# Kernel optimization log

Hardware: AMD Instinct MI355X
Metric: run time of the kernel (lower is better)

Reference implementation:

```python
import jax, jax.numpy as jnp
import numpy as np

NEG_INF = -9e15
ALPHA = 0.2  # LeakyReLU negative slope

N, IN_F, OUT_F = 8192, 512, 64


def setup_inputs() -> dict:
    key = jax.random.key(0)
    k1, k2, k3, k4 = jax.random.split(key, 4)
    input = jax.random.normal(k1, (N, IN_F), dtype=jnp.float32)
    adj = jax.random.randint(k2, (N, N), 0, 2, dtype=jnp.int32)
    init_range = float(np.sqrt(6.0 / (IN_F + OUT_F)))
    W = jax.random.uniform(k3, (IN_F, OUT_F), dtype=jnp.float32,
                           minval=-init_range, maxval=init_range)
    a_range = float(np.sqrt(6.0 / (2 * OUT_F + 1)))
    a = jax.random.uniform(k4, (2 * OUT_F, 1), dtype=jnp.float32,
                           minval=-a_range, maxval=a_range)
    return {"input": input, "adj": adj, "W": W, "a": a}


def reference(input, adj, W, a):
    h = input @ W                      # [N, F']
    a_left, a_right = a[:OUT_F], a[OUT_F:]   # each [F', 1]
    att_l = h @ a_left                 # [N, 1]
    att_r = h @ a_right                # [N, 1]
    e = jax.nn.leaky_relu(att_l + att_r.T, negative_slope=ALPHA)  # [N, N]
    e = jnp.where(adj == 0, jnp.float32(NEG_INF), e)
    attention = jax.nn.softmax(e, axis=1)
    # dropout is identity in eval mode (training=False)
    h_prime = attention @ h            # [N, F']
    return jax.nn.elu(h_prime)         # concat=True -> ELU activation
```

## Files before the change

kernel.cpp:

```cpp
#include <hip/hip_runtime.h>
#include <stdint.h>

#define ALPHA 0.2f
#define LOG2E 1.44269504088896340736f

typedef __attribute__((ext_vector_type(8))) short bf16x8;
typedef __attribute__((ext_vector_type(4))) float f32x4;

__device__ __forceinline__ unsigned short f2bf(float f) {
    unsigned u = __builtin_bit_cast(unsigned, f);
    u += 0x7fffu + ((u >> 16) & 1u);
    return (unsigned short)(u >> 16);
}
__device__ __forceinline__ float bf2f(unsigned short h) {
    unsigned u = ((unsigned)h) << 16;
    return __builtin_bit_cast(float, u);
}
__device__ __forceinline__ unsigned f2ord(float f) {
    unsigned b = __builtin_bit_cast(unsigned, f);
    return (b & 0x80000000u) ? ~b : (b | 0x80000000u);
}
__device__ __forceinline__ float ord2f(unsigned k) {
    unsigned b = (k & 0x80000000u) ? (k & 0x7fffffffu) : ~k;
    return __builtin_bit_cast(float, b);
}

__global__ __launch_bounds__(256) void gat_h(
    const float* __restrict__ input, const float* __restrict__ W,
    float* __restrict__ h)
{
    __shared__ float x_lds[16 * 128];
    const int tid = threadIdx.x;
    const int i0  = (blockIdx.x >> 2) * 16;
    const int k0  = (blockIdx.x & 3) * 128;

    {
        const int r  = tid >> 4;
        const int jc = (tid & 15) * 8;
        const float* src = input + (size_t)(i0 + r) * 512 + k0 + jc;
        *(f32x4*)&x_lds[r * 128 + jc]     = *(const f32x4*)src;
        *(f32x4*)&x_lds[r * 128 + jc + 4] = *(const f32x4*)(src + 4);
    }
    __syncthreads();

    const int c = tid & 63;
    const int w = tid >> 6;
    float acc[4] = {0.f, 0.f, 0.f, 0.f};
    const float* Wc = W + (size_t)k0 * 64 + c;
    #pragma unroll 4
    for (int kk = 0; kk < 128; kk += 4) {
        const float w0 = Wc[(kk+0)*64], w1 = Wc[(kk+1)*64];
        const float w2 = Wc[(kk+2)*64], w3 = Wc[(kk+3)*64];
        #pragma unroll
        for (int ri = 0; ri < 4; ++ri) {
            const f32x4 x = *(const f32x4*)&x_lds[(w + 4*ri) * 128 + kk];
            acc[ri] += x.x * w0 + x.y * w1 + x.z * w2 + x.w * w3;
        }
    }
    #pragma unroll
    for (int ri = 0; ri < 4; ++ri)
        unsafeAtomicAdd(&h[(size_t)(i0 + w + 4*ri) * 64 + c], acc[ri]);
}

__global__ __launch_bounds__(256) void gat_aux(
    const float* __restrict__ h, const float* __restrict__ a,
    float* __restrict__ attL, float* __restrict__ attR,
    unsigned short* __restrict__ hPack, unsigned* __restrict__ wsR)
{
    __shared__ float hl[32 * 64];
    __shared__ unsigned rmax;
    const int tid = threadIdx.x;
    const int j0  = blockIdx.x * 32;
    if (tid == 0) rmax = 0u;

    {
        const float* src = h + (size_t)j0 * 64 + tid * 8;
        *(f32x4*)&hl[tid * 8]     = *(const f32x4*)src;
        *(f32x4*)&hl[tid * 8 + 4] = *(const f32x4*)(src + 4);
    }
    __syncthreads();

    {
        const int row = tid >> 3;
        const int cs  = (tid & 7) * 8;
        float pL = 0.f, pR = 0.f;
        #pragma unroll
        for (int u = 0; u < 8; ++u) {
            const float hv = hl[row * 64 + cs + u];
            pL += hv * a[cs + u];
            pR += hv * a[64 + cs + u];
        }
        pL += __shfl_xor(pL, 1, 64); pR += __shfl_xor(pR, 1, 64);
        pL += __shfl_xor(pL, 2, 64); pR += __shfl_xor(pR, 2, 64);
        pL += __shfl_xor(pL, 4, 64); pR += __shfl_xor(pR, 4, 64);
        if ((tid & 7) == 0) {
            attL[j0 + row] = pL;
            attR[j0 + row] = pR;
            atomicMax(&rmax, f2ord(pR));
        }
    }

    {
        const int g = tid >> 6;
        const int l = tid & 63;
        const int m = l & 15;
        const int q = l >> 4;
        bf16x8 v;
        #pragma unroll
        for (int u = 0; u < 8; ++u)
            v[u] = (short)f2bf(hl[(q * 8 + u) * 64 + g * 16 + m]);
        *(bf16x8*)&hPack[(size_t)(blockIdx.x * 4 + g) * 512 + l * 8] = v;
    }

    __syncthreads();
    if (tid == 0) atomicMax(wsR, rmax);
}

__global__ __launch_bounds__(256, 8) void gat_attn(
    const int* __restrict__ adj,
    const float* __restrict__ attL, const float* __restrict__ attR,
    const unsigned short* __restrict__ hPack, const unsigned* __restrict__ wsR,
    float* __restrict__ outAcc, float* __restrict__ lAcc)
{
    __shared__ unsigned smem[4096];
    __shared__ float l_lds[64];
    const int tid  = threadIdx.x;
    const int lane = tid & 63;
    const int wq   = tid >> 6;
    const int m    = lane & 15;
    const int quad = lane >> 4;
    const int ti   = blockIdx.x >> 2;
    const int q4   = blockIdx.x & 3;
    const int i0   = ti * 16;
    const int jc0  = q4 * 64 + wq * 16;

    {
        const int r    = tid >> 4;
        const int lidx = (tid & 3) * 16 + r;
        const int t    = (tid & 15) >> 2;
        unsigned char* bb = (unsigned char*)smem;
        const int* src = adj + (size_t)(i0 + r) * 8192 + q4 * 2048 + (tid & 15) * 8;
        #pragma unroll 4
        for (int it = 0; it < 16; ++it) {
            const int4 v0 = *(const int4*)(src + it * 128);
            const int4 v1 = *(const int4*)(src + it * 128 + 4);
            unsigned b = 0;
            b |= (v0.x != 0) << 0; b |= (v0.y != 0) << 1;
            b |= (v0.z != 0) << 2; b |= (v0.w != 0) << 3;
            b |= (v1.x != 0) << 4; b |= (v1.y != 0) << 5;
            b |= (v1.z != 0) << 6; b |= (v1.w != 0) << 7;
            bb[((((it >> 2) * 1024) + (it & 3) * 64 + lidx) << 2) + t] = (unsigned char)b;
        }
    }
    __syncthreads();

    unsigned abw[4];
    #pragma unroll
    for (int g4 = 0; g4 < 4; ++g4)
        abw[g4] = smem[wq * 1024 + g4 * 64 + lane];

    const float R   = ord2f(*wsR);
    const float a_l = attL[i0 + m];
    const float t0  = a_l + R;
    const float M   = fmaxf(t0, ALPHA * t0);
    const float mc  = M * LOG2E;

    const float*          ar_p = attR + jc0 * 32 + quad * 8;
    const unsigned short* hp_p = hPack + (size_t)jc0 * 4 * 512 + lane * 8;

    f32x4 acc[4];
    #pragma unroll
    for (int g = 0; g < 4; ++g) acc[g] = (f32x4){0.f, 0.f, 0.f, 0.f};
    float lsum = 0.f;

    #pragma unroll
    for (int jg = 0; jg < 4; ++jg) {
        const unsigned ab = abw[jg];
        #pragma unroll
        for (int t = 0; t < 4; ++t) {
            const int s = jg * 4 + t;
            const f32x4 r0 = *(const f32x4*)(ar_p + s * 32);
            const f32x4 r1 = *(const f32x4*)(ar_p + s * 32 + 4);
            bf16x8 B[4];
            #pragma unroll
            for (int g = 0; g < 4; ++g)
                B[g] = *(const bf16x8*)(hp_p + (size_t)(s * 4 + g) * 512);

            const unsigned bits = (ab >> (t * 8)) & 0xffu;
            const float tv[8] = { a_l + r0.x, a_l + r0.y, a_l + r0.z, a_l + r0.w,
                                  a_l + r1.x, a_l + r1.y, a_l + r1.z, a_l + r1.w };
            bf16x8 af;
            #pragma unroll
            for (int u = 0; u < 8; ++u) {
                const float e  = fmaxf(tv[u], ALPHA * tv[u]);
                const float pe = __builtin_amdgcn_exp2f(__builtin_fmaf(e, LOG2E, -mc));
                const float pv = (bits & (1u << u)) ? pe : 0.0f;
                const unsigned short pb = f2bf(pv);
                af[u] = (short)pb;
                lsum += bf2f(pb);
            }
            #pragma unroll
            for (int g = 0; g < 4; ++g)
                acc[g] = __builtin_amdgcn_mfma_f32_16x16x32_bf16(af, B[g], acc[g], 0, 0, 0);
        }
    }

    lsum += __shfl_xor(lsum, 16, 64);
    lsum += __shfl_xor(lsum, 32, 64);
    if (lane < 16) l_lds[wq * 16 + lane] = lsum;
    float* accf = (float*)smem;
    #pragma unroll
    for (int g = 0; g < 4; ++g)
        *(f32x4*)&accf[(wq * 64 + lane) * 16 + g * 4] = acc[g];
    __syncthreads();

    #pragma unroll
    for (int q = 0; q < 4; ++q) {
        const int e      = tid + q * 256;
        const int lane_e = e >> 4;
        const int k16    = e & 15;
        float s = 0.f;
        #pragma unroll
        for (int ww = 0; ww < 4; ++ww) s += accf[(ww * 64 + lane_e) * 16 + k16];
        const int row = (lane_e >> 4) * 4 + (k16 & 3);
        const int col = (k16 >> 2) * 16 + (lane_e & 15);
        unsafeAtomicAdd(&outAcc[(size_t)(i0 + row) * 64 + col], s);
    }
    if (tid < 16) {
        const float s = l_lds[tid] + l_lds[16 + tid] + l_lds[32 + tid] + l_lds[48 + tid];
        unsafeAtomicAdd(&lAcc[i0 + tid], s);
    }
}

__global__ __launch_bounds__(256) void gat_final(
    float* __restrict__ out, const float* __restrict__ lAcc)
{
    const int idx = blockIdx.x * 256 + threadIdx.x;
    const float v = out[idx] / lAcc[idx >> 6];
    out[idx] = v > 0.f ? v : (__builtin_amdgcn_exp2f(v * LOG2E) - 1.0f);
}

extern "C" void kernel_launch(void* const* d_in, const int* in_sizes, int n_in,
                              void* d_out, int out_size, void* d_ws, size_t ws_size,
                              hipStream_t stream) {
    const float* input = (const float*)d_in[0];
    const int*   adj   = (const int*)d_in[1];
    const float* W     = (const float*)d_in[2];
    const float* a     = (const float*)d_in[3];
    float* out = (float*)d_out;

    char* ws = (char*)d_ws;
    unsigned*       wsR   = (unsigned*)(ws + 0);
    float*          lAcc  = (float*)(ws + 4096);
    float*          h     = (float*)(ws + 36864);
    float*          attL  = (float*)(ws + 2134016);
    float*          attR  = (float*)(ws + 2166784);
    unsigned short* hPack = (unsigned short*)(ws + 2199552);

    hipMemsetAsync(d_out, 0, (size_t)out_size * sizeof(float), stream);
    hipMemsetAsync(d_ws, 0, 2134016, stream);

    gat_h    <<<2048, 256, 0, stream>>>(input, W, h);
    gat_aux  <<< 256, 256, 0, stream>>>(h, a, attL, attR, hPack, wsR);
    gat_attn <<<2048, 256, 0, stream>>>(adj, attL, attR, hPack, wsR, out, lAcc);
    gat_final<<<2048, 256, 0, stream>>>(out, lAcc);
}
```

Before: 415.4 us.

## Factor attention exponentials and replace atomic accumulations with partial buffers

Since exp is monotonic, exp(leakyrelu(l+r)-M) is rewritten as max(exp(l-M)·exp(r), exp(0.2l-M)·exp(0.2r)). Per-column exponentials are precomputed in the aux kernel, so the attention inner loop does two multiplies and a max instead of an exp per element. Atomic adds for h, the output and the row sums are replaced by per-split partial buffers that later kernels reduce, which also removes the large memsets. Adjacency bit packing now uses shifted adds, assuming entries are 0 or 1. The factored exps may overflow for large attention logits.

```diff
diff --git a/kernel.cpp b/kernel.cpp
--- a/kernel.cpp
+++ b/kernel.cpp
@@ -27,12 +27,13 @@
 
 __global__ __launch_bounds__(256) void gat_h(
     const float* __restrict__ input, const float* __restrict__ W,
-    float* __restrict__ h)
+    float* __restrict__ hPart)
 {
     __shared__ float x_lds[16 * 128];
     const int tid = threadIdx.x;
     const int i0  = (blockIdx.x >> 2) * 16;
-    const int k0  = (blockIdx.x & 3) * 128;
+    const int ks  = blockIdx.x & 3;
+    const int k0  = ks * 128;
 
     {
         const int r  = tid >> 4;
@@ -59,12 +60,12 @@
     }
     #pragma unroll
     for (int ri = 0; ri < 4; ++ri)
-        unsafeAtomicAdd(&h[(size_t)(i0 + w + 4*ri) * 64 + c], acc[ri]);
+        hPart[((size_t)ks * 8192 + i0 + w + 4*ri) * 64 + c] = acc[ri];
 }
 
 __global__ __launch_bounds__(256) void gat_aux(
-    const float* __restrict__ h, const float* __restrict__ a,
-    float* __restrict__ attL, float* __restrict__ attR,
+    const float* __restrict__ hPart, const float* __restrict__ a,
+    float* __restrict__ attL, float* __restrict__ ERt, float* __restrict__ ER2t,
     unsigned short* __restrict__ hPack, unsigned* __restrict__ wsR)
 {
     __shared__ float hl[32 * 64];
@@ -74,9 +75,19 @@
     if (tid == 0) rmax = 0u;
 
     {
-        const float* src = h + (size_t)j0 * 64 + tid * 8;
-        *(f32x4*)&hl[tid * 8]     = *(const f32x4*)src;
-        *(f32x4*)&hl[tid * 8 + 4] = *(const f32x4*)(src + 4);
+        const size_t base = (size_t)j0 * 64 + tid * 8;
+        f32x4 s0 = *(const f32x4*)&hPart[base];
+        f32x4 s1 = *(const f32x4*)&hPart[base + 4];
+        #pragma unroll
+        for (int ks = 1; ks < 4; ++ks) {
+            const size_t o = (size_t)ks * 524288 + base;
+            const f32x4 u0 = *(const f32x4*)&hPart[o];
+            const f32x4 u1 = *(const f32x4*)&hPart[o + 4];
+            s0.x += u0.x; s0.y += u0.y; s0.z += u0.z; s0.w += u0.w;
+            s1.x += u1.x; s1.y += u1.y; s1.z += u1.z; s1.w += u1.w;
+        }
+        *(f32x4*)&hl[tid * 8]     = s0;
+        *(f32x4*)&hl[tid * 8 + 4] = s1;
     }
     __syncthreads();
 
@@ -95,7 +106,8 @@
         pL += __shfl_xor(pL, 4, 64); pR += __shfl_xor(pR, 4, 64);
         if ((tid & 7) == 0) {
             attL[j0 + row] = pL;
-            attR[j0 + row] = pR;
+            ERt [j0 + row] = __builtin_amdgcn_exp2f(pR * LOG2E);
+            ER2t[j0 + row] = __builtin_amdgcn_exp2f(ALPHA * pR * LOG2E);
             atomicMax(&rmax, f2ord(pR));
         }
     }
@@ -118,9 +130,10 @@
 
 __global__ __launch_bounds__(256, 8) void gat_attn(
     const int* __restrict__ adj,
-    const float* __restrict__ attL, const float* __restrict__ attR,
+    const float* __restrict__ attL, const float* __restrict__ ERt,
+    const float* __restrict__ ER2t,
     const unsigned short* __restrict__ hPack, const unsigned* __restrict__ wsR,
-    float* __restrict__ outAcc, float* __restrict__ lAcc)
+    float* __restrict__ pOut, float* __restrict__ lPart)
 {
     __shared__ unsigned smem[4096];
     __shared__ float l_lds[64];
@@ -144,11 +157,10 @@
         for (int it = 0; it < 16; ++it) {
             const int4 v0 = *(const int4*)(src + it * 128);
             const int4 v1 = *(const int4*)(src + it * 128 + 4);
-            unsigned b = 0;
-            b |= (v0.x != 0) << 0; b |= (v0.y != 0) << 1;
-            b |= (v0.z != 0) << 2; b |= (v0.w != 0) << 3;
-            b |= (v1.x != 0) << 4; b |= (v1.y != 0) << 5;
-            b |= (v1.z != 0) << 6; b |= (v1.w != 0) << 7;
+            const unsigned b = (unsigned)v0.x + ((unsigned)v0.y << 1)
+                             + ((unsigned)v0.z << 2) + ((unsigned)v0.w << 3)
+                             + ((unsigned)v1.x << 4) + ((unsigned)v1.y << 5)
+                             + ((unsigned)v1.z << 6) + ((unsigned)v1.w << 7);
             bb[((((it >> 2) * 1024) + (it & 3) * 64 + lidx) << 2) + t] = (unsigned char)b;
         }
     }
@@ -164,9 +176,12 @@
     const float t0  = a_l + R;
     const float M   = fmaxf(t0, ALPHA * t0);
     const float mc  = M * LOG2E;
-
-    const float*          ar_p = attR + jc0 * 32 + quad * 8;
-    const unsigned short* hp_p = hPack + (size_t)jc0 * 4 * 512 + lane * 8;
+    const float EL  = __builtin_amdgcn_exp2f(__builtin_fmaf(a_l, LOG2E, -mc));
+    const float EL2 = __builtin_amdgcn_exp2f(__builtin_fmaf(ALPHA * a_l, LOG2E, -mc));
+
+    const float*          er_p  = ERt  + jc0 * 32 + quad * 8;
+    const float*          er2_p = ER2t + jc0 * 32 + quad * 8;
+    const unsigned short* hp_p  = hPack + (size_t)jc0 * 4 * 512 + lane * 8;
 
     f32x4 acc[4];
     #pragma unroll
@@ -179,22 +194,23 @@
         #pragma unroll
         for (int t = 0; t < 4; ++t) {
             const int s = jg * 4 + t;
-            const f32x4 r0 = *(const f32x4*)(ar_p + s * 32);
-            const f32x4 r1 = *(const f32x4*)(ar_p + s * 32 + 4);
+            const f32x4 e0  = *(const f32x4*)(er_p  + s * 32);
+            const f32x4 e1  = *(const f32x4*)(er_p  + s * 32 + 4);
+            const f32x4 f0  = *(const f32x4*)(er2_p + s * 32);
+            const f32x4 f1  = *(const f32x4*)(er2_p + s * 32 + 4);
             bf16x8 B[4];
             #pragma unroll
             for (int g = 0; g < 4; ++g)
                 B[g] = *(const bf16x8*)(hp_p + (size_t)(s * 4 + g) * 512);
 
             const unsigned bits = (ab >> (t * 8)) & 0xffu;
-            const float tv[8] = { a_l + r0.x, a_l + r0.y, a_l + r0.z, a_l + r0.w,
-                                  a_l + r1.x, a_l + r1.y, a_l + r1.z, a_l + r1.w };
+            const float ev[8] = { e0.x, e0.y, e0.z, e0.w, e1.x, e1.y, e1.z, e1.w };
+            const float fv[8] = { f0.x, f0.y, f0.z, f0.w, f1.x, f1.y, f1.z, f1.w };
             bf16x8 af;
             #pragma unroll
             for (int u = 0; u < 8; ++u) {
-                const float e  = fmaxf(tv[u], ALPHA * tv[u]);
-                const float pe = __builtin_amdgcn_exp2f(__builtin_fmaf(e, LOG2E, -mc));
-                const float pv = (bits & (1u << u)) ? pe : 0.0f;
+                const float p  = fmaxf(EL * ev[u], EL2 * fv[u]);
+                const float pv = (bits & (1u << u)) ? p : 0.0f;
                 const unsigned short pb = f2bf(pv);
                 af[u] = (short)pb;
                 lsum += bf2f(pb);
@@ -224,20 +240,26 @@
         for (int ww = 0; ww < 4; ++ww) s += accf[(ww * 64 + lane_e) * 16 + k16];
         const int row = (lane_e >> 4) * 4 + (k16 & 3);
         const int col = (k16 >> 2) * 16 + (lane_e & 15);
-        unsafeAtomicAdd(&outAcc[(size_t)(i0 + row) * 64 + col], s);
+        pOut[((size_t)q4 * 8192 + i0 + row) * 64 + col] = s;
     }
     if (tid < 16) {
-        const float s = l_lds[tid] + l_lds[16 + tid] + l_lds[32 + tid] + l_lds[48 + tid];
-        unsafeAtomicAdd(&lAcc[i0 + tid], s);
+        lPart[q4 * 8192 + i0 + tid] =
+            l_lds[tid] + l_lds[16 + tid] + l_lds[32 + tid] + l_lds[48 + tid];
     }
 }
 
 __global__ __launch_bounds__(256) void gat_final(
-    float* __restrict__ out, const float* __restrict__ lAcc)
+    const float* __restrict__ pOut, const float* __restrict__ lPart,
+    float* __restrict__ out)
 {
     const int idx = blockIdx.x * 256 + threadIdx.x;
-    const float v = out[idx] / lAcc[idx >> 6];
-    out[idx] = v > 0.f ? v : (__builtin_amdgcn_exp2f(v * LOG2E) - 1.0f);
+    const int row = idx >> 6;
+    const float v = pOut[idx] + pOut[524288 + idx] + pOut[1048576 + idx]
+                  + pOut[1572864 + idx];
+    const float l = lPart[row] + lPart[8192 + row] + lPart[16384 + row]
+                  + lPart[24576 + row];
+    const float r = v / l;
+    out[idx] = r > 0.f ? r : (__builtin_amdgcn_exp2f(r * LOG2E) - 1.0f);
 }
 
 extern "C" void kernel_launch(void* const* d_in, const int* in_sizes, int n_in,
@@ -251,17 +273,18 @@
 
     char* ws = (char*)d_ws;
     unsigned*       wsR   = (unsigned*)(ws + 0);
-    float*          lAcc  = (float*)(ws + 4096);
-    float*          h     = (float*)(ws + 36864);
-    float*          attL  = (float*)(ws + 2134016);
-    float*          attR  = (float*)(ws + 2166784);
-    unsigned short* hPack = (unsigned short*)(ws + 2199552);
-
-    hipMemsetAsync(d_out, 0, (size_t)out_size * sizeof(float), stream);
-    hipMemsetAsync(d_ws, 0, 2134016, stream);
-
-    gat_h    <<<2048, 256, 0, stream>>>(input, W, h);
-    gat_aux  <<< 256, 256, 0, stream>>>(h, a, attL, attR, hPack, wsR);
-    gat_attn <<<2048, 256, 0, stream>>>(adj, attL, attR, hPack, wsR, out, lAcc);
-    gat_final<<<2048, 256, 0, stream>>>(out, lAcc);
-}
+    float*          attL  = (float*)(ws + 4096);
+    float*          ERt   = (float*)(ws + 36864);
+    float*          ER2t  = (float*)(ws + 69632);
+    float*          lPart = (float*)(ws + 102400);
+    unsigned short* hPack = (unsigned short*)(ws + 262144);
+    float*          hPart = (float*)(ws + 2097152);
+    float*          pOut  = (float*)(ws + 10485760);
+
+    hipMemsetAsync(d_ws, 0, 64, stream);
+
+    gat_h    <<<2048, 256, 0, stream>>>(input, W, hPart);
+    gat_aux  <<< 256, 256, 0, stream>>>(hPart, a, attL, ERt, ER2t, hPack, wsR);
+    gat_attn <<<2048, 256, 0, stream>>>(adj, attL, ERt, ER2t, hPack, wsR, pOut, lPart);
+    gat_final<<<2048, 256, 0, stream>>>(pOut, lPart, out);
+}
```

Result: slower. 437.4 us (+5.3%).
